# Optimization experiments

Hardware: AMD Instinct MI355X
Metric: run time of the kernel (lower is better)

Reference implementation:

```python
import jax, jax.numpy as jnp
import numpy as np
import math

D_MODEL = 1024
N_HEADS = 16
HEAD_DIM = D_MODEL // N_HEADS
SEQ_LEN = 8192
INCLUDE_LOCAL = 2


def get_dilated_positions(seq_len, include_local=2):
    # Faithful numpy port of the torch pattern generator (runs once at setup).
    max_attend = include_local + int(math.ceil(math.log2(seq_len + 1)))
    positions = np.zeros((seq_len, max_attend), dtype=np.int64)
    mask = np.zeros((seq_len, max_attend), dtype=bool)
    for i in range(seq_len):
        ap = [i]
        for j in range(1, include_local + 1):
            if i - j >= 0:
                ap.append(i - j)
        k = 2
        while i - 2 ** k >= 0:
            ap.append(i - 2 ** k)
            k += 1
        positions[i, :len(ap)] = ap
        mask[i, :len(ap)] = True
    return positions, mask


def setup_inputs() -> dict:
    key = jax.random.key(0)
    kx, kq, kk, kv, ko = jax.random.split(key, 5)
    x = jax.random.normal(kx, (1, SEQ_LEN, D_MODEL), dtype=jnp.float32)
    # nn.Linear(bias=False) weights, torch layout [out_features, in_features]
    s = 0.02
    q_w = jax.random.normal(kq, (D_MODEL, D_MODEL), dtype=jnp.float32) * s
    k_w = jax.random.normal(kk, (D_MODEL, D_MODEL), dtype=jnp.float32) * s
    v_w = jax.random.normal(kv, (D_MODEL, D_MODEL), dtype=jnp.float32) * s
    o_w = jax.random.normal(ko, (D_MODEL, D_MODEL), dtype=jnp.float32) * s
    pos_np, mask_np = get_dilated_positions(SEQ_LEN, INCLUDE_LOCAL)
    return {
        "x": x,
        "q_w": q_w, "k_w": k_w, "v_w": v_w, "o_w": o_w,
        "positions": jnp.asarray(pos_np),   # (S, A) int64 indices
        "attend_mask": jnp.asarray(mask_np) # (S, A) bool
    }


def reference(x, q_w, k_w, v_w, o_w, positions, attend_mask):
    B, S, _ = x.shape
    H, Dh = N_HEADS, HEAD_DIM
    scale = Dh ** -0.5

    q = (x @ q_w.T).reshape(B, S, H, Dh).transpose(0, 2, 1, 3)  # (B,H,S,Dh)
    k = (x @ k_w.T).reshape(B, S, H, Dh).transpose(0, 2, 1, 3)
    v = (x @ v_w.T).reshape(B, S, H, Dh).transpose(0, 2, 1, 3)

    # Gather K/V at the dilated positions: (B,H,S,A,Dh)
    k_sparse = k[:, :, positions, :]
    v_sparse = v[:, :, positions, :]

    scores = jnp.einsum('bhsd,bhsad->bhsa', q, k_sparse) * scale
    scores = jnp.where(attend_mask[None, None, :, :], scores, -jnp.inf)
    attn = jax.nn.softmax(scores, axis=-1)  # dropout p in eval / 0.0 -> identity

    out = jnp.einsum('bhsa,bhsad->bhsd', attn, v_sparse)
    out = out.transpose(0, 2, 1, 3).reshape(B, S, D_MODEL)
    return out @ o_w.T
```

## Files before the change

kernel.cpp:

```cpp
#include <hip/hip_runtime.h>
#include <hip/hip_bf16.h>

typedef __bf16 bf16_t;
typedef __bf16 bf16x4 __attribute__((ext_vector_type(4)));
typedef __bf16 bf16x8 __attribute__((ext_vector_type(8)));
typedef float floatx16 __attribute__((ext_vector_type(16)));

#define SEQ    8192
#define DM     1024
#define NHEADS 16
#define HDIM   64

__device__ __forceinline__ void async_ld16(bf16_t* lds, const bf16_t* g) {
  __builtin_amdgcn_global_load_lds(
      (__attribute__((address_space(1))) void*)g,
      (__attribute__((address_space(3))) void*)lds, 16, 0, 0);
}

__global__ __launch_bounds__(256)
void cvt_all(const float* __restrict__ x,  const float* __restrict__ qw,
             const float* __restrict__ kw, const float* __restrict__ vw,
             const float* __restrict__ ow,
             bf16_t* __restrict__ Xb,  bf16_t* __restrict__ QWb,
             bf16_t* __restrict__ KWb, bf16_t* __restrict__ VWb,
             bf16_t* __restrict__ OWb) {
  const int b = blockIdx.x;
  const float* in; bf16_t* out; int g;
  if (b < 8192) { in = x; out = Xb; g = b; }
  else {
    const int w  = (b - 8192) >> 10;
    const int wb = (b - 8192) & 1023;
    switch (w) {
      case 0:  in = qw; out = QWb; break;
      case 1:  in = kw; out = KWb; break;
      case 2:  in = vw; out = VWb; break;
      default: in = ow; out = OWb; break;
    }
    g = wb;
  }
  const int idx = (g * 256 + threadIdx.x) * 4;
  float4 v = *(const float4*)(in + idx);
  bf16x4 o = { (bf16_t)v.x, (bf16_t)v.y, (bf16_t)v.z, (bf16_t)v.w };
  *(bf16x4*)(out + idx) = o;
}

template <typename OutT>
__device__ __forceinline__ void gemm128_core(
    const bf16_t* __restrict__ A, const bf16_t* __restrict__ B,
    OutT* __restrict__ C, float scl)
{
  constexpr int Kdim = DM;
  __shared__ __attribute__((aligned(16))) bf16_t sA[128 * 64];
  __shared__ __attribute__((aligned(16))) bf16_t sB[128 * 64];

  const int tid  = threadIdx.x;
  const int wave = tid >> 6;
  const int lane = tid & 63;
  const int l31  = lane & 31;
  const int half = lane >> 5;
  const int wr   = (wave >> 1) * 64;
  const int wc   = (wave & 1) * 64;

  const int gc = (lane & 7) ^ ((lane >> 3) & 7);
  const size_t arow0 = (size_t)blockIdx.x * 128 + wave * 32 + (lane >> 3);
  const size_t brow0 = (size_t)blockIdx.y * 128 + wave * 32 + (lane >> 3);
  const bf16_t* Ag = A + arow0 * Kdim + gc * 8;
  const bf16_t* Bg = B + brow0 * Kdim + gc * 8;
  bf16_t* sAw = sA + wave * 32 * 64;
  bf16_t* sBw = sB + wave * 32 * 64;

  floatx16 acc[2][2];
  #pragma unroll
  for (int i = 0; i < 2; ++i)
    #pragma unroll
    for (int j = 0; j < 2; ++j)
      acc[i][j] = (floatx16)(0.0f);

  const int sw = l31 & 7;

  for (int ko = 0; ko < Kdim; ko += 64) {
    #pragma unroll
    for (int n = 0; n < 4; ++n) {
      async_ld16(sAw + n * 512, Ag + (size_t)n * 8 * Kdim + ko);
      async_ld16(sBw + n * 512, Bg + (size_t)n * 8 * Kdim + ko);
    }
    __syncthreads();

    #pragma unroll
    for (int s = 0; s < 4; ++s) {
      const int ck   = s * 2 + half;
      const int slot = (ck ^ sw) * 8;
      bf16x8 af[2], bfr[2];
      #pragma unroll
      for (int mi = 0; mi < 2; ++mi)
        af[mi] = *(const bf16x8*)&sA[(wr + mi * 32 + l31) * 64 + slot];
      #pragma unroll
      for (int ni = 0; ni < 2; ++ni)
        bfr[ni] = *(const bf16x8*)&sB[(wc + ni * 32 + l31) * 64 + slot];

      #pragma unroll
      for (int mi = 0; mi < 2; ++mi)
        #pragma unroll
        for (int ni = 0; ni < 2; ++ni)
          acc[mi][ni] = __builtin_amdgcn_mfma_f32_32x32x16_bf16(af[mi], bfr[ni], acc[mi][ni], 0, 0, 0);
    }

    __syncthreads();
  }

  const int crow0 = blockIdx.x * 128 + wr + 4 * half;
  const int ccol0 = blockIdx.y * 128 + wc + l31;
  #pragma unroll
  for (int mi = 0; mi < 2; ++mi)
    #pragma unroll
    for (int ni = 0; ni < 2; ++ni)
      #pragma unroll
      for (int r = 0; r < 16; ++r) {
        const int row = crow0 + mi * 32 + (r & 3) + 8 * (r >> 2);
        C[(size_t)row * DM + (ccol0 + ni * 32)] = (OutT)(acc[mi][ni][r] * scl);
      }
}

__global__ __launch_bounds__(256)
void gemm_proj(const bf16_t* __restrict__ A, const bf16_t* __restrict__ B,
               bf16_t* __restrict__ C, float scl)
{
  gemm128_core<bf16_t>(A, B, C, scl);
}

__global__ __launch_bounds__(256)
void gemm_outk(const bf16_t* __restrict__ A, const bf16_t* __restrict__ B,
               float* __restrict__ C)
{
  gemm128_core<float>(A, B, C, 1.0f);
}

__global__ __launch_bounds__(512)
void dilated_attn(const bf16_t* __restrict__ Q, const bf16_t* __restrict__ K,
                  const bf16_t* __restrict__ V, bf16_t* O)
{
  __shared__ float sM[3][2][64];
  __shared__ float sL[3][2][64];
  __shared__ float sAcc[3][2][64][17];

  const int lane = threadIdx.x & 63;
  const int wv   = threadIdx.x >> 6;
  const int ql   = wv >> 2;
  const int sub  = wv & 3;
  const int qb   = (blockIdx.x & 7) * 512 + (blockIdx.x >> 3);
  const int i    = qb * 2 + ql;
  const size_t base = (size_t)i * DM + lane * 16;

  bf16x8 q0 = *(const bf16x8*)(Q + base);
  bf16x8 q1 = *(const bf16x8*)(Q + base + 8);
  float qf[16];
  #pragma unroll
  for (int j = 0; j < 8; ++j) { qf[j] = (float)q0[j]; qf[j + 8] = (float)q1[j]; }

  const int npos = (i == 0) ? 1 : (33 - __builtin_clz((unsigned)i));
  auto pos_addr = [&](int t) -> size_t {
    const int off = (t == 0) ? 0 : (1 << (t - 1));
    return (size_t)(i - off) * DM + lane * 16;
  };

  float m = -INFINITY, l = 0.0f;
  float acc[16];
  #pragma unroll
  for (int j = 0; j < 16; ++j) acc[j] = 0.0f;

  int t = sub;
  if (t < npos) {
    size_t a = pos_addr(t);
    bf16x8 k0 = *(const bf16x8*)(K + a), k1 = *(const bf16x8*)(K + a + 8);
    bf16x8 v0 = *(const bf16x8*)(V + a), v1 = *(const bf16x8*)(V + a + 8);
    while (true) {
      const int tn = t + 4;
      const bool more = (tn < npos);
      bf16x8 nk0, nk1, nv0, nv1;
      if (more) {
        const size_t na = pos_addr(tn);
        nk0 = *(const bf16x8*)(K + na); nk1 = *(const bf16x8*)(K + na + 8);
        nv0 = *(const bf16x8*)(V + na); nv1 = *(const bf16x8*)(V + na + 8);
      }

      float sc = 0.0f;
      #pragma unroll
      for (int j = 0; j < 8; ++j) sc += qf[j] * (float)k0[j] + qf[j + 8] * (float)k1[j];
      sc += __shfl_xor(sc, 1, 64);
      sc += __shfl_xor(sc, 2, 64);

      float mn = fmaxf(m, sc);
      float co = __expf(m - mn);
      float w  = __expf(sc - mn);
      l = l * co + w;
      m = mn;
      #pragma unroll
      for (int j = 0; j < 8; ++j) {
        acc[j]     = acc[j]     * co + w * (float)v0[j];
        acc[j + 8] = acc[j + 8] * co + w * (float)v1[j];
      }

      if (!more) break;
      k0 = nk0; k1 = nk1; v0 = nv0; v1 = nv1;
      t = tn;
    }
  }

  if (sub != 0) {
    sM[sub - 1][ql][lane] = m;
    sL[sub - 1][ql][lane] = l;
    #pragma unroll
    for (int j = 0; j < 16; ++j) sAcc[sub - 1][ql][lane][j] = acc[j];
  }
  __syncthreads();
  if (sub == 0) {
    #pragma unroll
    for (int p = 0; p < 3; ++p) {
      const float mb = sM[p][ql][lane], lb = sL[p][ql][lane];
      const float mt = fmaxf(m, mb);
      const float ca = __expf(m - mt);
      const float cb = __expf(mb - mt);
      l = l * ca + lb * cb;
      #pragma unroll
      for (int j = 0; j < 16; ++j)
        acc[j] = acc[j] * ca + sAcc[p][ql][lane][j] * cb;
      m = mt;
    }
    const float inv = 1.0f / l;
    bf16x8 o0, o1;
    #pragma unroll
    for (int j = 0; j < 8; ++j) {
      o0[j] = (bf16_t)(acc[j]     * inv);
      o1[j] = (bf16_t)(acc[j + 8] * inv);
    }
    *(bf16x8*)(O + base)     = o0;
    *(bf16x8*)(O + base + 8) = o1;
  }
}

extern "C" void kernel_launch(void* const* d_in, const int* in_sizes, int n_in,
                              void* d_out, int out_size, void* d_ws, size_t ws_size,
                              hipStream_t stream) {
  (void)in_sizes; (void)n_in; (void)out_size; (void)ws_size;
  const float* x  = (const float*)d_in[0];
  const float* qw = (const float*)d_in[1];
  const float* kw = (const float*)d_in[2];
  const float* vw = (const float*)d_in[3];
  const float* ow = (const float*)d_in[4];
  float* out = (float*)d_out;

  bf16_t* Xb  = (bf16_t*)d_ws;
  bf16_t* Qb  = Xb  + (size_t)SEQ * DM;
  bf16_t* Kb  = Qb  + (size_t)SEQ * DM;
  bf16_t* Vb  = Kb  + (size_t)SEQ * DM;
  bf16_t* QWb = Vb  + (size_t)SEQ * DM;
  bf16_t* KWb = QWb + (size_t)DM * DM;
  bf16_t* VWb = KWb + (size_t)DM * DM;
  bf16_t* OWb = VWb + (size_t)DM * DM;
  bf16_t* AO  = Qb;

  cvt_all<<<dim3(8192 + 4096), dim3(256), 0, stream>>>(x, qw, kw, vw, ow,
                                                       Xb, QWb, KWb, VWb, OWb);

  dim3 pg(SEQ / 128, DM / 128);
  gemm_proj<<<pg, dim3(256), 0, stream>>>(Xb, QWb, Qb, 0.125f);
  gemm_proj<<<pg, dim3(256), 0, stream>>>(Xb, KWb, Kb, 1.0f);
  gemm_proj<<<pg, dim3(256), 0, stream>>>(Xb, VWb, Vb, 1.0f);
  dilated_attn<<<dim3(SEQ / 2), dim3(512), 0, stream>>>(Qb, Kb, Vb, AO);
  gemm_outk<<<pg, dim3(256), 0, stream>>>(AO, OWb, out);
}
```

Baseline: 226.4 us.

## Process each query in one wave with dual softmax streams, dropping LDS merge

The attention kernel now gives each query row to a single wave instead of four cooperating waves, so the shared-memory partial merge and the block barrier go away. Each wave keeps two independent online-softmax accumulators (even and odd positions) and double-buffers the K/V loads two positions ahead to keep memory requests in flight. The block remap groups 4 queries per block and interleaves chunks across blocks. In exchange each wave walks the full position list serially, which lengthens the per-query latency chain and raises register pressure.

```diff
diff --git a/kernel.cpp b/kernel.cpp
--- a/kernel.cpp
+++ b/kernel.cpp
@@ -135,20 +135,16 @@
   gemm128_core<float>(A, B, C, 1.0f);
 }
 
-__global__ __launch_bounds__(512)
+__global__ __launch_bounds__(256)
 void dilated_attn(const bf16_t* __restrict__ Q, const bf16_t* __restrict__ K,
                   const bf16_t* __restrict__ V, bf16_t* O)
 {
-  __shared__ float sM[3][2][64];
-  __shared__ float sL[3][2][64];
-  __shared__ float sAcc[3][2][64][17];
-
   const int lane = threadIdx.x & 63;
   const int wv   = threadIdx.x >> 6;
-  const int ql   = wv >> 2;
-  const int sub  = wv & 3;
-  const int qb   = (blockIdx.x & 7) * 512 + (blockIdx.x >> 3);
-  const int i    = qb * 2 + ql;
+  const int bid  = blockIdx.x;
+  const int jj   = bid >> 3;
+  const int chunk= (bid & 7) + ((jj >> 6) << 3);
+  const int i    = chunk * 256 + (jj & 63) * 4 + wv;
   const size_t base = (size_t)i * DM + lane * 16;
 
   bf16x8 q0 = *(const bf16x8*)(Q + base);
@@ -162,80 +158,72 @@
     const int off = (t == 0) ? 0 : (1 << (t - 1));
     return (size_t)(i - off) * DM + lane * 16;
   };
-
-  float m = -INFINITY, l = 0.0f;
-  float acc[16];
-  #pragma unroll
-  for (int j = 0; j < 16; ++j) acc[j] = 0.0f;
-
-  int t = sub;
-  if (t < npos) {
-    size_t a = pos_addr(t);
-    bf16x8 k0 = *(const bf16x8*)(K + a), k1 = *(const bf16x8*)(K + a + 8);
-    bf16x8 v0 = *(const bf16x8*)(V + a), v1 = *(const bf16x8*)(V + a + 8);
-    while (true) {
-      const int tn = t + 4;
-      const bool more = (tn < npos);
-      bf16x8 nk0, nk1, nv0, nv1;
-      if (more) {
-        const size_t na = pos_addr(tn);
-        nk0 = *(const bf16x8*)(K + na); nk1 = *(const bf16x8*)(K + na + 8);
-        nv0 = *(const bf16x8*)(V + na); nv1 = *(const bf16x8*)(V + na + 8);
-      }
-
-      float sc = 0.0f;
-      #pragma unroll
-      for (int j = 0; j < 8; ++j) sc += qf[j] * (float)k0[j] + qf[j + 8] * (float)k1[j];
-      sc += __shfl_xor(sc, 1, 64);
-      sc += __shfl_xor(sc, 2, 64);
-
-      float mn = fmaxf(m, sc);
-      float co = __expf(m - mn);
-      float w  = __expf(sc - mn);
-      l = l * co + w;
-      m = mn;
-      #pragma unroll
-      for (int j = 0; j < 8; ++j) {
-        acc[j]     = acc[j]     * co + w * (float)v0[j];
-        acc[j + 8] = acc[j + 8] * co + w * (float)v1[j];
-      }
-
-      if (!more) break;
-      k0 = nk0; k1 = nk1; v0 = nv0; v1 = nv1;
-      t = tn;
-    }
-  }
-
-  if (sub != 0) {
-    sM[sub - 1][ql][lane] = m;
-    sL[sub - 1][ql][lane] = l;
-    #pragma unroll
-    for (int j = 0; j < 16; ++j) sAcc[sub - 1][ql][lane][j] = acc[j];
-  }
-  __syncthreads();
-  if (sub == 0) {
-    #pragma unroll
-    for (int p = 0; p < 3; ++p) {
-      const float mb = sM[p][ql][lane], lb = sL[p][ql][lane];
-      const float mt = fmaxf(m, mb);
-      const float ca = __expf(m - mt);
-      const float cb = __expf(mb - mt);
-      l = l * ca + lb * cb;
-      #pragma unroll
-      for (int j = 0; j < 16; ++j)
-        acc[j] = acc[j] * ca + sAcc[p][ql][lane][j] * cb;
-      m = mt;
-    }
-    const float inv = 1.0f / l;
-    bf16x8 o0, o1;
+  auto ld_pos = [&](int t, bf16x8& k0, bf16x8& k1, bf16x8& v0, bf16x8& v1) {
+    const size_t a = pos_addr(t);
+    k0 = *(const bf16x8*)(K + a); k1 = *(const bf16x8*)(K + a + 8);
+    v0 = *(const bf16x8*)(V + a); v1 = *(const bf16x8*)(V + a + 8);
+  };
+
+  float mE = -INFINITY, lE = 0.0f, mD = -INFINITY, lD = 0.0f;
+  float aE[16], aD[16];
+  #pragma unroll
+  for (int j = 0; j < 16; ++j) { aE[j] = 0.0f; aD[j] = 0.0f; }
+
+  auto step = [&](float& m, float& l, float* acc,
+                  const bf16x8& k0, const bf16x8& k1,
+                  const bf16x8& v0, const bf16x8& v1) {
+    float sc = 0.0f;
+    #pragma unroll
+    for (int j = 0; j < 8; ++j) sc += qf[j] * (float)k0[j] + qf[j + 8] * (float)k1[j];
+    sc += __shfl_xor(sc, 1, 64);
+    sc += __shfl_xor(sc, 2, 64);
+    const float mn = fmaxf(m, sc);
+    const float co = __expf(m - mn);
+    const float w  = __expf(sc - mn);
+    l = l * co + w;
+    m = mn;
     #pragma unroll
     for (int j = 0; j < 8; ++j) {
-      o0[j] = (bf16_t)(acc[j]     * inv);
-      o1[j] = (bf16_t)(acc[j + 8] * inv);
-    }
-    *(bf16x8*)(O + base)     = o0;
-    *(bf16x8*)(O + base + 8) = o1;
-  }
+      acc[j]     = acc[j]     * co + w * (float)v0[j];
+      acc[j + 8] = acc[j + 8] * co + w * (float)v1[j];
+    }
+  };
+
+  bf16x8 xk0a, xk1a, xv0a, xv1a, xk0b, xk1b, xv0b, xv1b;
+  bf16x8 yk0a, yk1a, yv0a, yv1a, yk0b, yk1b, yv0b, yv1b;
+
+  ld_pos(0, xk0a, xk1a, xv0a, xv1a);
+  if (1 < npos) ld_pos(1, xk0b, xk1b, xv0b, xv1b);
+
+  for (int t = 0; ; t += 4) {
+    const bool pe1 = (t + 2) < npos;
+    if (pe1)            ld_pos(t + 2, yk0a, yk1a, yv0a, yv1a);
+    const bool pd1 = (t + 3) < npos;
+    if (pd1)            ld_pos(t + 3, yk0b, yk1b, yv0b, yv1b);
+    step(mE, lE, aE, xk0a, xk1a, xv0a, xv1a);
+    if ((t + 1) < npos) step(mD, lD, aD, xk0b, xk1b, xv0b, xv1b);
+    if (!pe1) break;
+
+    const bool pe2 = (t + 4) < npos;
+    if (pe2)            ld_pos(t + 4, xk0a, xk1a, xv0a, xv1a);
+    if ((t + 5) < npos) ld_pos(t + 5, xk0b, xk1b, xv0b, xv1b);
+    step(mE, lE, aE, yk0a, yk1a, yv0a, yv1a);
+    if (pd1)            step(mD, lD, aD, yk0b, yk1b, yv0b, yv1b);
+    if (!pe2) break;
+  }
+
+  const float mt = fmaxf(mE, mD);
+  const float ca = __expf(mE - mt);
+  const float cb = __expf(mD - mt);
+  const float inv = 1.0f / (lE * ca + lD * cb);
+  bf16x8 o0, o1;
+  #pragma unroll
+  for (int j = 0; j < 8; ++j) {
+    o0[j] = (bf16_t)((aE[j]     * ca + aD[j]     * cb) * inv);
+    o1[j] = (bf16_t)((aE[j + 8] * ca + aD[j + 8] * cb) * inv);
+  }
+  *(bf16x8*)(O + base)     = o0;
+  *(bf16x8*)(O + base + 8) = o1;
 }
 
 extern "C" void kernel_launch(void* const* d_in, const int* in_sizes, int n_in,
@@ -266,6 +254,6 @@
   gemm_proj<<<pg, dim3(256), 0, stream>>>(Xb, QWb, Qb, 0.125f);
   gemm_proj<<<pg, dim3(256), 0, stream>>>(Xb, KWb, Kb, 1.0f);
   gemm_proj<<<pg, dim3(256), 0, stream>>>(Xb, VWb, Vb, 1.0f);
-  dilated_attn<<<dim3(SEQ / 2), dim3(512), 0, stream>>>(Qb, Kb, Vb, AO);
+  dilated_attn<<<dim3(SEQ / 4), dim3(256), 0, stream>>>(Qb, Kb, Vb, AO);
   gemm_outk<<<pg, dim3(256), 0, stream>>>(AO, OWb, out);
 }
```

Result: no change. 224.2 us, median of 2 (-1.0%).
